# Optimization experiments

Measured on AMD Instinct MI355X. Metric: run time of the kernel, lower is better.

Reference implementation:

```python
import jax, jax.numpy as jnp
import numpy as np

B, N, S, K, NDIM, HID = 2, 8192, 1024, 32, 3, 256


def _sincos_embed(pos, dim):
    # pos: (..., ndim) continuous coordinates -> (..., dim) sincos embedding
    ndim = pos.shape[-1]
    emb_dim_per_dim = dim // ndim
    half = emb_dim_per_dim // 2
    freq = jnp.exp(jnp.arange(half, dtype=pos.dtype) * (-np.log(10000.0) / (half - 1)))
    embs = []
    for i in range(ndim):
        e = pos[..., i:i + 1] * freq  # (..., half)
        embs.append(jnp.concatenate([jnp.sin(e), jnp.cos(e)], axis=-1))
    x = jnp.concatenate(embs, axis=-1)  # (..., ndim*2*half)
    pad = dim - x.shape[-1]
    if pad > 0:
        x = jnp.pad(x, [(0, 0)] * (x.ndim - 1) + [(0, pad)])
    return x


def setup_inputs() -> dict:
    key = jax.random.key(0)
    ks = jax.random.split(key, 8)
    input_pos = jax.random.normal(ks[0], (B, N, NDIM), dtype=jnp.float32)
    supernode_idxs = jax.random.randint(ks[1], (S,), 0, N)
    # lecun_normal-style init (stddev = 1/sqrt(fan_in)), zero bias (torch/flax Dense default bias=0)
    w_in = jax.random.normal(ks[2], (NDIM, HID), dtype=jnp.float32) / np.sqrt(NDIM)
    b_in = jnp.zeros((HID,), jnp.float32)
    w1 = jax.random.normal(ks[3], (HID, HID), dtype=jnp.float32) / np.sqrt(HID)
    b1 = jnp.zeros((HID,), jnp.float32)
    w2 = jax.random.normal(ks[4], (HID, HID), dtype=jnp.float32) / np.sqrt(HID)
    b2 = jnp.zeros((HID,), jnp.float32)
    return {"input_pos": input_pos, "supernode_idxs": supernode_idxs,
            "w_in": w_in, "b_in": b_in, "w1": w1, "b1": b1, "w2": w2, "b2": b2}


def reference(input_pos, supernode_idxs, w_in, b_in, w1, b1, w2, b2):
    def knn(x):  # x: (N, ndim)
        # Euclidean distance from each supernode to every point: (S, N).
        # Same values as rows of the full NxN cdist the original materializes.
        d = jnp.sqrt(jnp.sum((x[supernode_idxs][:, None, :] - x[None, :, :]) ** 2, axis=-1))
        nbr = jnp.argsort(d, axis=1)[:, :K]  # (S, K)
        return x[nbr]  # (S, K, ndim)

    coords = jax.vmap(knn)(input_pos)  # (B, S, K, ndim)
    proj = coords @ w_in + b_in                         # (B, S, K, HID)
    pe = _sincos_embed(coords, HID)                     # (B, S, K, HID)
    h = proj + pe
    h = jax.nn.gelu(h @ w1 + b1) @ w2 + b2              # message MLP
    return jnp.mean(h, axis=-2)                         # (B, S, HID)
```

## Files before the change

### kernel.cpp

```cpp
#include <hip/hip_runtime.h>
#include <hip/hip_bf16.h>
#include <math.h>

#define BB   2
#define NN   8192
#define SS   1024
#define KK   32
#define HID  256
#define NTH  256
#define PPT  32
#define SENT 0xFFFFFFFFFFFFFFFFULL
#define LDB  264
#define WFE  65536

typedef unsigned long long u64;
typedef unsigned int       u32;
typedef short bf16x8 __attribute__((ext_vector_type(8)));
typedef float f32x4  __attribute__((ext_vector_type(4)));

#define CSW(SI) { const u64 mn = x < (SI) ? x : (SI); const u64 mx = x < (SI) ? (SI) : x; (SI) = mn; x = mx; }
#define INS(KV) { u64 x = (KV); CSW(s0) CSW(s1) CSW(s2) CSW(s3) }

__device__ __forceinline__ float tanh_fast(float y) {
    const float e = __expf(2.0f * y);
    const float r = __builtin_amdgcn_rcpf(e + 1.0f);
    return fmaf(-2.0f, r, 1.0f);
}

__device__ __forceinline__ short bf_bits(float f) {
    const __hip_bfloat16 h = __float2bfloat16(f);
    short s;
    __builtin_memcpy(&s, &h, 2);
    return s;
}

__device__ __forceinline__ int mbcnt64(u64 m) {
    return (int)__builtin_amdgcn_mbcnt_hi((u32)(m >> 32),
           __builtin_amdgcn_mbcnt_lo((u32)m, 0u));
}

__global__ void prep_w(const float* __restrict__ w1, const float* __restrict__ w2,
                       __hip_bfloat16* __restrict__ wf) {
    const int idx = blockIdx.x * 256 + threadIdx.x;
    const int mat = idx >> 16;
    const int e   = idx & (WFE - 1);
    const int j   = e & 7;
    const int l   = (e >> 3) & 63;
    const int ks  = (e >> 9) & 7;
    const int ntg = e >> 12;
    const int k = ks * 32 + (l >> 4) * 8 + j;
    const int n = ntg * 16 + (l & 15);
    const float v = (mat ? w2 : w1)[k * HID + n];
    const __hip_bfloat16 hi = __float2bfloat16(v);
    const float res = v - __bfloat162float(hi);
    wf[(size_t)mat * 2 * WFE + e]       = hi;
    wf[(size_t)mat * 2 * WFE + WFE + e] = __float2bfloat16(res);
}

__global__ __launch_bounds__(NTH, 8)
void snp_kernel(const float* __restrict__ pos,
                const int*   __restrict__ snidx,
                const float* __restrict__ w_in,
                const float* __restrict__ b_in,
                const float* __restrict__ b1,
                const float* __restrict__ b2,
                const __hip_bfloat16* __restrict__ wf,
                float*       __restrict__ out)
{
    const int bs   = blockIdx.x;
    const int b    = bs / SS;
    const int s    = bs - b * SS;
    const int t    = threadIdx.x;
    const int lane = t & 63;
    const int wv   = t >> 6;

    __shared__ __align__(16) short h0b[KK][LDB];
    __shared__ u64   wl[4 * KK];
    __shared__ int   nbr[KK];
    __shared__ float nbc[3 * KK];

    const float* posb = pos + (size_t)b * (NN * 3);
    const int   sp = snidx[s];
    const float sx = posb[sp*3 + 0];
    const float sy = posb[sp*3 + 1];
    const float sz = posb[sp*3 + 2];

    u64 s0=SENT,s1=SENT,s2=SENT,s3=SENT;
#pragma unroll 4
    for (int c = 0; c < PPT; ++c) {
        const int i = c * NTH + t;
        const float dx = __fsub_rn(sx, posb[i*3 + 0]);
        const float dy = __fsub_rn(sy, posb[i*3 + 1]);
        const float dz = __fsub_rn(sz, posb[i*3 + 2]);
        const float sq = __fadd_rn(__fadd_rn(__fmul_rn(dx,dx), __fmul_rn(dy,dy)),
                                   __fmul_rn(dz,dz));
        const u64 kv = ((u64)__float_as_uint(__fsqrt_rn(sq)) << 13) | (u32)i;
        INS(kv);
    }

    {
        u64 L = 0;
        for (int bit = 43; bit >= 0; --bit) {
            const u64 cand = L | (1ull << bit);
            const int cnt = __popcll(__ballot(s0 < cand)) + __popcll(__ballot(s1 < cand))
                          + __popcll(__ballot(s2 < cand)) + __popcll(__ballot(s3 < cand));
            if (cnt < 32) L = cand;
        }
        const bool b0 = s0 <= L, b1 = s1 <= L, b2 = s2 <= L, b3 = s3 <= L;
        const int csel = (int)b0 + (int)b1 + (int)b2 + (int)b3;

        if (__ballot(csel == 4) != 0ull) {
            int nv = 4;
#pragma unroll 1
            for (int it = 0; it < KK; ++it) {
                u64 m = s0;
#pragma unroll
                for (int off = 32; off > 0; off >>= 1) {
                    const u64 o = __shfl_xor(m, off, 64);
                    m = o < m ? o : m;
                }
                if (lane == 0) wl[wv*KK + it] = m;
                if (s0 == m) {
                    s0=s1; s1=s2; s2=s3; s3=SENT;
                    if (--nv == 0) {
                        const u64 last = m;
                        s0=s1=s2=s3=SENT;
#pragma unroll 4
                        for (int c = 0; c < PPT; ++c) {
                            const int i = c * NTH + t;
                            const float dx = __fsub_rn(sx, posb[i*3 + 0]);
                            const float dy = __fsub_rn(sy, posb[i*3 + 1]);
                            const float dz = __fsub_rn(sz, posb[i*3 + 2]);
                            const float sq = __fadd_rn(__fadd_rn(__fmul_rn(dx,dx), __fmul_rn(dy,dy)),
                                                       __fmul_rn(dz,dz));
                            u64 kv = ((u64)__float_as_uint(__fsqrt_rn(sq)) << 13) | (u32)i;
                            kv = kv > last ? kv : SENT;
                            INS(kv);
                        }
                        nv = (int)(s0!=SENT)+(int)(s1!=SENT)+(int)(s2!=SENT)+(int)(s3!=SENT);
                    }
                }
            }
        } else {
            const u64 m0 = __ballot(b0), m1 = __ballot(b1),
                      m2 = __ballot(b2), m3 = __ballot(b3);
            const int pos = mbcnt64(m0) + mbcnt64(m1) + mbcnt64(m2) + mbcnt64(m3);
            u64* wwl = &wl[wv * KK];
            if (b0) wwl[pos]     = s0;
            if (b1) wwl[pos + 1] = s1;
            if (b2) wwl[pos + 2] = s2;
            if (b3) wwl[pos + 3] = s3;
        }
    }
    __syncthreads();

    if (t < 64) {
        const u64 k0 = wl[lane], k1 = wl[64 + lane];
        u64 L = 0;
        for (int bit = 43; bit >= 0; --bit) {
            const u64 cand = L | (1ull << bit);
            const int cnt = __popcll(__ballot(k0 < cand)) + __popcll(__ballot(k1 < cand));
            if (cnt < 32) L = cand;
        }
        const bool c0 = k0 <= L, c1 = k1 <= L;
        const int p = mbcnt64(__ballot(c0)) + mbcnt64(__ballot(c1));
        if (c0) nbr[p]            = (int)(k0 & 8191u);
        if (c1) nbr[p + (int)c0]  = (int)(k1 & 8191u);
    }
    __syncthreads();

    if (t < KK * 3) {
        nbc[t] = posb[(size_t)nbr[t / 3] * 3 + (t % 3)];
    }
    __syncthreads();

    {
        const int  c     = t;
        const int  dimi  = c / 84;
        const int  cc    = c - dimi * 84;
        const bool hasPe = c < 252;
        const bool isCos = cc >= 42;
        const int  f     = isCos ? cc - 42 : cc;
        const float fcoef = (float)(-9.210340371976184 / 41.0);
        const float freqv = expf((float)f * fcoef);
        const int  di    = hasPe ? dimi : 0;

        const float wi0 = w_in[0*HID + c];
        const float wi1 = w_in[1*HID + c];
        const float wi2 = w_in[2*HID + c];
        const float bi  = b_in[c];

#pragma unroll 4
        for (int k = 0; k < KK; ++k) {
            const float x0 = nbc[3*k+0], x1 = nbc[3*k+1], x2 = nbc[3*k+2];
            float v = fmaf(x2, wi2, fmaf(x1, wi1, fmaf(x0, wi0, bi)));
            if (hasPe) {
                const float xv  = (di == 0) ? x0 : ((di == 1) ? x1 : x2);
                const float ang = xv * freqv;
                v += isCos ? __cosf(ang) : __sinf(ang);
            }
            h0b[k][c] = bf_bits(v);
        }
    }
    __syncthreads();

    const int lr = lane & 15;
    const int lg = lane >> 4;
    const int nbase = wv * 64;

    f32x4 acc[2][4];

    {
        const __hip_bfloat16* wh  = wf;
        const __hip_bfloat16* wlo = wf + WFE;
#pragma unroll
        for (int nt = 0; nt < 4; ++nt) {
            const float bias = b1[nbase + nt*16 + lr];
            const f32x4 bv = {bias, bias, bias, bias};
            acc[0][nt] = bv; acc[1][nt] = bv;
        }
#pragma unroll 1
        for (int ks = 0; ks < 8; ++ks) {
            const int k0 = ks * 32 + lg * 8;
            const bf16x8 af0 = *(const bf16x8*)&h0b[lr][k0];
            const bf16x8 af1 = *(const bf16x8*)&h0b[16 + lr][k0];
#pragma unroll
            for (int nt = 0; nt < 4; ++nt) {
                const size_t off = ((size_t)((wv*4 + nt)*8 + ks) * 64 + lane) * 8;
                {
                    const bf16x8 bh = *(const bf16x8*)(wh + off);
                    acc[0][nt] = __builtin_amdgcn_mfma_f32_16x16x32_bf16(af0, bh, acc[0][nt], 0,0,0);
                    acc[1][nt] = __builtin_amdgcn_mfma_f32_16x16x32_bf16(af1, bh, acc[1][nt], 0,0,0);
                }
                {
                    const bf16x8 bl = *(const bf16x8*)(wlo + off);
                    acc[0][nt] = __builtin_amdgcn_mfma_f32_16x16x32_bf16(af0, bl, acc[0][nt], 0,0,0);
                    acc[1][nt] = __builtin_amdgcn_mfma_f32_16x16x32_bf16(af1, bl, acc[1][nt], 0,0,0);
                }
            }
        }
    }
    __syncthreads();

    {
        const float kA = 0.7978845608028654f;
#pragma unroll
        for (int mt = 0; mt < 2; ++mt)
#pragma unroll
        for (int nt = 0; nt < 4; ++nt)
#pragma unroll
        for (int r = 0; r < 4; ++r) {
            const float x  = acc[mt][nt][r];
            const float x3 = x * x * x;
            const float tv = tanh_fast(kA * fmaf(0.044715f, x3, x));
            h0b[mt*16 + lg*4 + r][nbase + nt*16 + lr] = bf_bits(0.5f * x * (1.0f + tv));
        }
    }
    __syncthreads();

    {
        const __hip_bfloat16* wh  = wf + 2*WFE;
        const __hip_bfloat16* wlo = wf + 3*WFE;
        const f32x4 z = {0.f, 0.f, 0.f, 0.f};
#pragma unroll
        for (int nt = 0; nt < 4; ++nt) { acc[0][nt] = z; acc[1][nt] = z; }
#pragma unroll 1
        for (int ks = 0; ks < 8; ++ks) {
            const int k0 = ks * 32 + lg * 8;
            const bf16x8 af0 = *(const bf16x8*)&h0b[lr][k0];
            const bf16x8 af1 = *(const bf16x8*)&h0b[16 + lr][k0];
#pragma unroll
            for (int nt = 0; nt < 4; ++nt) {
                const size_t off = ((size_t)((wv*4 + nt)*8 + ks) * 64 + lane) * 8;
                {
                    const bf16x8 bh = *(const bf16x8*)(wh + off);
                    acc[0][nt] = __builtin_amdgcn_mfma_f32_16x16x32_bf16(af0, bh, acc[0][nt], 0,0,0);
                    acc[1][nt] = __builtin_amdgcn_mfma_f32_16x16x32_bf16(af1, bh, acc[1][nt], 0,0,0);
                }
                {
                    const bf16x8 bl = *(const bf16x8*)(wlo + off);
                    acc[0][nt] = __builtin_amdgcn_mfma_f32_16x16x32_bf16(af0, bl, acc[0][nt], 0,0,0);
                    acc[1][nt] = __builtin_amdgcn_mfma_f32_16x16x32_bf16(af1, bl, acc[1][nt], 0,0,0);
                }
            }
        }
    }

#pragma unroll
    for (int nt = 0; nt < 4; ++nt) {
        float ssum = 0.0f;
#pragma unroll
        for (int mt = 0; mt < 2; ++mt)
#pragma unroll
            for (int r = 0; r < 4; ++r) ssum += acc[mt][nt][r];
        ssum += __shfl_xor(ssum, 16, 64);
        ssum += __shfl_xor(ssum, 32, 64);
        if (lane < 16) {
            const int ch = nbase + nt*16 + lane;
            out[(size_t)bs * HID + ch] = fmaf(ssum, 1.0f / KK, b2[ch]);
        }
    }
}

extern "C" void kernel_launch(void* const* d_in, const int* in_sizes, int n_in,
                              void* d_out, int out_size, void* d_ws, size_t ws_size,
                              hipStream_t stream) {
    const float* pos  = (const float*)d_in[0];
    const int*   sni  = (const int*)  d_in[1];
    const float* w_in = (const float*)d_in[2];
    const float* b_in = (const float*)d_in[3];
    const float* w1   = (const float*)d_in[4];
    const float* b1   = (const float*)d_in[5];
    const float* w2   = (const float*)d_in[6];
    const float* b2   = (const float*)d_in[7];
    float* out = (float*)d_out;
    __hip_bfloat16* wf = (__hip_bfloat16*)d_ws;
    (void)ws_size; (void)in_sizes; (void)n_in; (void)out_size;

    hipLaunchKernelGGL(prep_w, dim3(2 * WFE / 256), dim3(256), 0, stream, w1, w2, wf);
    hipLaunchKernelGGL(snp_kernel, dim3(BB * SS), dim3(NTH), 0, stream,
                       pos, sni, w_in, b_in, b1, b2, wf, out);
}
```

Measured before the change: 88.85 us.

## Interleave split-bf16 weight fragments, shorten radix select, pad neighbor coords

Reorders the pre-split bf16 weight layout so that, for each k-step, the high and low fragments of all column tiles sit next to each other, and simplifies the address arithmetic in both MFMA loops. The radix-select threshold search now tests only the distance bits first. It resolves the 13 index bits only when the count does not land on exactly 32. Neighbor coordinates are padded to 4 floats so each can be read with one float4 LDS load. These changes aim to cut ballot iterations, integer address math and scattered global weight loads, at the cost of more code complexity in the selection path.

Measured after the change: 86.57 us. 2.6% less time.

```diff
diff --git a/kernel.cpp b/kernel.cpp
--- a/kernel.cpp
+++ b/kernel.cpp
@@ -42,19 +42,19 @@
 __global__ void prep_w(const float* __restrict__ w1, const float* __restrict__ w2,
                        __hip_bfloat16* __restrict__ wf) {
     const int idx = blockIdx.x * 256 + threadIdx.x;
+    const int j   = idx & 7;
+    const int l   = (idx >> 3) & 63;
+    const int ntg = (idx >> 9) & 15;
+    const int ks  = (idx >> 13) & 7;
     const int mat = idx >> 16;
-    const int e   = idx & (WFE - 1);
-    const int j   = e & 7;
-    const int l   = (e >> 3) & 63;
-    const int ks  = (e >> 9) & 7;
-    const int ntg = e >> 12;
     const int k = ks * 32 + (l >> 4) * 8 + j;
     const int n = ntg * 16 + (l & 15);
     const float v = (mat ? w2 : w1)[k * HID + n];
     const __hip_bfloat16 hi = __float2bfloat16(v);
     const float res = v - __bfloat162float(hi);
-    wf[(size_t)mat * 2 * WFE + e]       = hi;
-    wf[(size_t)mat * 2 * WFE + WFE + e] = __float2bfloat16(res);
+    const size_t s0 = (size_t)mat * 131072 + ((size_t)((ks*16 + ntg)*2) * 64 + l) * 8 + j;
+    wf[s0]       = hi;
+    wf[s0 + 512] = __float2bfloat16(res);
 }
 
 __global__ __launch_bounds__(NTH, 8)
@@ -77,7 +77,7 @@
     __shared__ __align__(16) short h0b[KK][LDB];
     __shared__ u64   wl[4 * KK];
     __shared__ int   nbr[KK];
-    __shared__ float nbc[3 * KK];
+    __shared__ __align__(16) float nbc[4 * KK];
 
     const float* posb = pos + (size_t)b * (NN * 3);
     const int   sp = snidx[s];
@@ -100,13 +100,27 @@
 
     {
         u64 L = 0;
-        for (int bit = 43; bit >= 0; --bit) {
+        for (int bit = 43; bit >= 13; --bit) {
             const u64 cand = L | (1ull << bit);
             const int cnt = __popcll(__ballot(s0 < cand)) + __popcll(__ballot(s1 < cand))
                           + __popcll(__ballot(s2 < cand)) + __popcll(__ballot(s3 < cand));
             if (cnt < 32) L = cand;
         }
-        const bool b0 = s0 <= L, b1 = s1 <= L, b2 = s2 <= L, b3 = s3 <= L;
+        u64 TH = L + (1ull << 13);
+        {
+            const int cnt = __popcll(__ballot(s0 < TH)) + __popcll(__ballot(s1 < TH))
+                          + __popcll(__ballot(s2 < TH)) + __popcll(__ballot(s3 < TH));
+            if (cnt != 32) {
+                for (int bit = 12; bit >= 0; --bit) {
+                    const u64 cand = L | (1ull << bit);
+                    const int c2 = __popcll(__ballot(s0 < cand)) + __popcll(__ballot(s1 < cand))
+                                 + __popcll(__ballot(s2 < cand)) + __popcll(__ballot(s3 < cand));
+                    if (c2 < 32) L = cand;
+                }
+                TH = L + 1;
+            }
+        }
+        const bool b0 = s0 < TH, b1 = s1 < TH, b2 = s2 < TH, b3 = s3 < TH;
         const int csel = (int)b0 + (int)b1 + (int)b2 + (int)b3;
 
         if (__ballot(csel == 4) != 0ull) {
@@ -144,12 +158,12 @@
         } else {
             const u64 m0 = __ballot(b0), m1 = __ballot(b1),
                       m2 = __ballot(b2), m3 = __ballot(b3);
-            const int pos = mbcnt64(m0) + mbcnt64(m1) + mbcnt64(m2) + mbcnt64(m3);
+            const int pos2 = mbcnt64(m0) + mbcnt64(m1) + mbcnt64(m2) + mbcnt64(m3);
             u64* wwl = &wl[wv * KK];
-            if (b0) wwl[pos]     = s0;
-            if (b1) wwl[pos + 1] = s1;
-            if (b2) wwl[pos + 2] = s2;
-            if (b3) wwl[pos + 3] = s3;
+            if (b0) wwl[pos2]     = s0;
+            if (b1) wwl[pos2 + 1] = s1;
+            if (b2) wwl[pos2 + 2] = s2;
+            if (b3) wwl[pos2 + 3] = s3;
         }
     }
     __syncthreads();
@@ -157,12 +171,24 @@
     if (t < 64) {
         const u64 k0 = wl[lane], k1 = wl[64 + lane];
         u64 L = 0;
-        for (int bit = 43; bit >= 0; --bit) {
+        for (int bit = 43; bit >= 13; --bit) {
             const u64 cand = L | (1ull << bit);
             const int cnt = __popcll(__ballot(k0 < cand)) + __popcll(__ballot(k1 < cand));
             if (cnt < 32) L = cand;
         }
-        const bool c0 = k0 <= L, c1 = k1 <= L;
+        u64 TH = L + (1ull << 13);
+        {
+            const int cnt = __popcll(__ballot(k0 < TH)) + __popcll(__ballot(k1 < TH));
+            if (cnt != 32) {
+                for (int bit = 12; bit >= 0; --bit) {
+                    const u64 cand = L | (1ull << bit);
+                    const int c2 = __popcll(__ballot(k0 < cand)) + __popcll(__ballot(k1 < cand));
+                    if (c2 < 32) L = cand;
+                }
+                TH = L + 1;
+            }
+        }
+        const bool c0 = k0 < TH, c1 = k1 < TH;
         const int p = mbcnt64(__ballot(c0)) + mbcnt64(__ballot(c1));
         if (c0) nbr[p]            = (int)(k0 & 8191u);
         if (c1) nbr[p + (int)c0]  = (int)(k1 & 8191u);
@@ -170,7 +196,8 @@
     __syncthreads();
 
     if (t < KK * 3) {
-        nbc[t] = posb[(size_t)nbr[t / 3] * 3 + (t % 3)];
+        const int k = t / 3, d = t - 3 * k;
+        nbc[k * 4 + d] = posb[(size_t)nbr[k] * 3 + d];
     }
     __syncthreads();
 
@@ -192,7 +219,8 @@
 
 #pragma unroll 4
         for (int k = 0; k < KK; ++k) {
-            const float x0 = nbc[3*k+0], x1 = nbc[3*k+1], x2 = nbc[3*k+2];
+            const float4 xv4 = *(const float4*)&nbc[k * 4];
+            const float x0 = xv4.x, x1 = xv4.y, x2 = xv4.z;
             float v = fmaf(x2, wi2, fmaf(x1, wi1, fmaf(x0, wi0, bi)));
             if (hasPe) {
                 const float xv  = (di == 0) ? x0 : ((di == 1) ? x1 : x2);
@@ -208,11 +236,14 @@
     const int lg = lane >> 4;
     const int nbase = wv * 64;
 
+    const short* arow0 = &h0b[lr][lg * 8];
+    const short* arow1 = &h0b[16 + lr][lg * 8];
+    const __hip_bfloat16* wb1 = wf + (size_t)wv * 4096 + lane * 8;
+    const __hip_bfloat16* wb2 = wb1 + 2 * WFE;
+
     f32x4 acc[2][4];
 
     {
-        const __hip_bfloat16* wh  = wf;
-        const __hip_bfloat16* wlo = wf + WFE;
 #pragma unroll
         for (int nt = 0; nt < 4; ++nt) {
             const float bias = b1[nbase + nt*16 + lr];
@@ -221,22 +252,17 @@
         }
 #pragma unroll 1
         for (int ks = 0; ks < 8; ++ks) {
-            const int k0 = ks * 32 + lg * 8;
-            const bf16x8 af0 = *(const bf16x8*)&h0b[lr][k0];
-            const bf16x8 af1 = *(const bf16x8*)&h0b[16 + lr][k0];
+            const bf16x8 af0 = *(const bf16x8*)(arow0 + ks * 32);
+            const bf16x8 af1 = *(const bf16x8*)(arow1 + ks * 32);
+            const __hip_bfloat16* p = wb1 + ks * 16384;
 #pragma unroll
             for (int nt = 0; nt < 4; ++nt) {
-                const size_t off = ((size_t)((wv*4 + nt)*8 + ks) * 64 + lane) * 8;
-                {
-                    const bf16x8 bh = *(const bf16x8*)(wh + off);
-                    acc[0][nt] = __builtin_amdgcn_mfma_f32_16x16x32_bf16(af0, bh, acc[0][nt], 0,0,0);
-                    acc[1][nt] = __builtin_amdgcn_mfma_f32_16x16x32_bf16(af1, bh, acc[1][nt], 0,0,0);
-                }
-                {
-                    const bf16x8 bl = *(const bf16x8*)(wlo + off);
-                    acc[0][nt] = __builtin_amdgcn_mfma_f32_16x16x32_bf16(af0, bl, acc[0][nt], 0,0,0);
-                    acc[1][nt] = __builtin_amdgcn_mfma_f32_16x16x32_bf16(af1, bl, acc[1][nt], 0,0,0);
-                }
+                const bf16x8 bh = *(const bf16x8*)(p + nt * 1024);
+                acc[0][nt] = __builtin_amdgcn_mfma_f32_16x16x32_bf16(af0, bh, acc[0][nt], 0,0,0);
+                acc[1][nt] = __builtin_amdgcn_mfma_f32_16x16x32_bf16(af1, bh, acc[1][nt], 0,0,0);
+                const bf16x8 bl = *(const bf16x8*)(p + nt * 1024 + 512);
+                acc[0][nt] = __builtin_amdgcn_mfma_f32_16x16x32_bf16(af0, bl, acc[0][nt], 0,0,0);
+                acc[1][nt] = __builtin_amdgcn_mfma_f32_16x16x32_bf16(af1, bl, acc[1][nt], 0,0,0);
             }
         }
     }
@@ -259,29 +285,22 @@
     __syncthreads();
 
     {
-        const __hip_bfloat16* wh  = wf + 2*WFE;
-        const __hip_bfloat16* wlo = wf + 3*WFE;
         const f32x4 z = {0.f, 0.f, 0.f, 0.f};
 #pragma unroll
         for (int nt = 0; nt < 4; ++nt) { acc[0][nt] = z; acc[1][nt] = z; }
 #pragma unroll 1
         for (int ks = 0; ks < 8; ++ks) {
-            const int k0 = ks * 32 + lg * 8;
-            const bf16x8 af0 = *(const bf16x8*)&h0b[lr][k0];
-            const bf16x8 af1 = *(const bf16x8*)&h0b[16 + lr][k0];
+            const bf16x8 af0 = *(const bf16x8*)(arow0 + ks * 32);
+            const bf16x8 af1 = *(const bf16x8*)(arow1 + ks * 32);
+            const __hip_bfloat16* p = wb2 + ks * 16384;
 #pragma unroll
             for (int nt = 0; nt < 4; ++nt) {
-                const size_t off = ((size_t)((wv*4 + nt)*8 + ks) * 64 + lane) * 8;
-                {
-                    const bf16x8 bh = *(const bf16x8*)(wh + off);
-                    acc[0][nt] = __builtin_amdgcn_mfma_f32_16x16x32_bf16(af0, bh, acc[0][nt], 0,0,0);
-                    acc[1][nt] = __builtin_amdgcn_mfma_f32_16x16x32_bf16(af1, bh, acc[1][nt], 0,0,0);
-                }
-                {
-                    const bf16x8 bl = *(const bf16x8*)(wlo + off);
-                    acc[0][nt] = __builtin_amdgcn_mfma_f32_16x16x32_bf16(af0, bl, acc[0][nt], 0,0,0);
-                    acc[1][nt] = __builtin_amdgcn_mfma_f32_16x16x32_bf16(af1, bl, acc[1][nt], 0,0,0);
-                }
+                const bf16x8 bh = *(const bf16x8*)(p + nt * 1024);
+                acc[0][nt] = __builtin_amdgcn_mfma_f32_16x16x32_bf16(af0, bh, acc[0][nt], 0,0,0);
+                acc[1][nt] = __builtin_amdgcn_mfma_f32_16x16x32_bf16(af1, bh, acc[1][nt], 0,0,0);
+                const bf16x8 bl = *(const bf16x8*)(p + nt * 1024 + 512);
+                acc[0][nt] = __builtin_amdgcn_mfma_f32_16x16x32_bf16(af0, bl, acc[0][nt], 0,0,0);
+                acc[1][nt] = __builtin_amdgcn_mfma_f32_16x16x32_bf16(af1, bl, acc[1][nt], 0,0,0);
             }
         }
     }
```
